# Kernel tuning notes

Measured on AMD Instinct MI355X. Metric: run time of the kernel, lower is better.

Reference implementation:

```python
import jax, jax.numpy as jnp
import numpy as np

N, F, H, O = 3072, 128, 16, 8  # nodes, in_channels, hidden_channels, out_channels


def setup_inputs() -> dict:
    key = jax.random.key(0)
    ks = jax.random.split(key, 8)
    s = 0.01  # xavier gain=0.01 in original init -> small weights
    return {
        "x": jax.random.normal(ks[0], (N, F), dtype=jnp.float32),
        "edge_index": jax.random.randint(ks[1], (2, N * 32), 0, N, dtype=jnp.int64),
        "node_distances": jax.random.uniform(ks[2], (N, N), dtype=jnp.float32),
        "normalization_matrix": jnp.ones((N, N), dtype=jnp.float32),
        # per-feature MLPs fs[f]: Linear(1,H) -> ReLU -> (Dropout p=0) -> Linear(H,O), stacked over F
        "W1": s * jax.random.normal(ks[3], (F, H), dtype=jnp.float32),
        "b1": jnp.zeros((F, H), dtype=jnp.float32),
        "W2": s * jax.random.normal(ks[4], (F, H, O), dtype=jnp.float32),
        "b2": jnp.zeros((F, O), dtype=jnp.float32),
        # rho MLP: Linear(1,H) -> ReLU -> Linear(H,O) (bias=True since is_graph_task=False)
        "rW1": s * jax.random.normal(ks[5], (H,), dtype=jnp.float32),
        "rb1": jnp.zeros((H,), dtype=jnp.float32),
        "rW2": s * jax.random.normal(ks[6], (H, O), dtype=jnp.float32),
        "rb2": jnp.zeros((O,), dtype=jnp.float32),
    }


def reference(x, edge_index, node_distances, normalization_matrix,
              W1, b1, W2, b2, rW1, rb1, rW2, rb2):
    # --- per-feature tiny MLPs, vectorized over the feature axis ---
    # h[n,f,:] = relu(x[n,f] * W1[f] + b1[f])
    h = jax.nn.relu(x[:, :, None] * W1[None, :, :] + b1[None, :, :])  # [N,F,H]
    fx = jnp.einsum('nfh,fho->nfo', h, W2) + b2[None, :, :]           # [N,F,O]
    # sum over features first (commutes with the matmul's F-reduction)
    g = fx.sum(axis=1)                                                 # [N,O]

    # --- rho MLP on normalized pairwise distances ---
    d = node_distances / normalization_matrix                          # [N,N]
    hd = jax.nn.relu(d[:, :, None] * rW1 + rb1)                        # [N,N,H]
    m = jnp.einsum('nmh,ho->nmo', hd, rW2) + rb2                       # [N,N,O]

    # out.T in torch: mf = m_dist_perm @ fx_perm summed over features -> [N,O]
    out = jnp.einsum('nmo,mo->no', m, g)                               # [N,O]
    return out
```

## Files before the change

kernel.cpp:

```cpp
#include <hip/hip_runtime.h>
#include <hip/hip_bf16.h>
#include <math.h>

#define NN 3072
#define FF 128
#define HH 16
#define OO 8

#define MC   1024
#define NCH  3
#define RPB  8

#define OFF_GT   0
#define OFF_KP   24576
#define OFF_ROWS 24600
#define OFF_REF  24872

#define NPB 4

__global__ __launch_bounds__(128) void gnan_g_kernel(
    const float* __restrict__ x,
    const float* __restrict__ W1,
    const float* __restrict__ b1,
    const float* __restrict__ W2,
    const float* __restrict__ b2,
    float* __restrict__ gT)
{
    const int f  = threadIdx.x;
    const int n0 = blockIdx.x * NPB;

    float xv[NPB];
#pragma unroll
    for (int ni = 0; ni < NPB; ++ni)
        xv[ni] = x[(size_t)(n0 + ni) * FF + f];

    const float4 b2a = *reinterpret_cast<const float4*>(b2 + f * OO);
    const float4 b2b = *reinterpret_cast<const float4*>(b2 + f * OO + 4);

    float acc[NPB][OO];
#pragma unroll
    for (int ni = 0; ni < NPB; ++ni) {
        acc[ni][0] = b2a.x; acc[ni][1] = b2a.y; acc[ni][2] = b2a.z; acc[ni][3] = b2a.w;
        acc[ni][4] = b2b.x; acc[ni][5] = b2b.y; acc[ni][6] = b2b.z; acc[ni][7] = b2b.w;
    }

    for (int h = 0; h < HH; ++h) {
        const float w1h = W1[f * HH + h];
        const float b1h = b1[f * HH + h];
        const float4 wa = *reinterpret_cast<const float4*>(W2 + (size_t)(f * HH + h) * OO);
        const float4 wb = *reinterpret_cast<const float4*>(W2 + (size_t)(f * HH + h) * OO + 4);
#pragma unroll
        for (int ni = 0; ni < NPB; ++ni) {
            const float a = fmaxf(fmaf(xv[ni], w1h, b1h), 0.f);
            acc[ni][0] = fmaf(a, wa.x, acc[ni][0]);
            acc[ni][1] = fmaf(a, wa.y, acc[ni][1]);
            acc[ni][2] = fmaf(a, wa.z, acc[ni][2]);
            acc[ni][3] = fmaf(a, wa.w, acc[ni][3]);
            acc[ni][4] = fmaf(a, wb.x, acc[ni][4]);
            acc[ni][5] = fmaf(a, wb.y, acc[ni][5]);
            acc[ni][6] = fmaf(a, wb.z, acc[ni][6]);
            acc[ni][7] = fmaf(a, wb.w, acc[ni][7]);
        }
    }

    __shared__ float wsum[2][OO];
    const int lane = threadIdx.x & 63;
    const int wid  = threadIdx.x >> 6;
#pragma unroll
    for (int ni = 0; ni < NPB; ++ni) {
#pragma unroll
        for (int o = 0; o < OO; ++o) {
#pragma unroll
            for (int off = 32; off > 0; off >>= 1)
                acc[ni][o] += __shfl_down(acc[ni][o], off);
        }
        if (lane == 0) {
#pragma unroll
            for (int o = 0; o < OO; ++o) wsum[wid][o] = acc[ni][o];
        }
        __syncthreads();
        if (threadIdx.x < OO)
            gT[threadIdx.x * NN + (n0 + ni)] = wsum[0][threadIdx.x] + wsum[1][threadIdx.x];
        __syncthreads();
    }
}

__global__ __launch_bounds__(256) void gnan_setup_kernel(
    const float* __restrict__ nd,
    const float* __restrict__ nm,
    const float* __restrict__ rW1,
    const float* __restrict__ rb1,
    const float* __restrict__ rW2,
    const float* __restrict__ rb2,
    float* __restrict__ wsf)
{
    const int t = threadIdx.x;

    float w[HH], b[HH], knee[HH];
#pragma unroll
    for (int h = 0; h < HH; ++h) {
        w[h] = rW1[h];
        b[h] = rb1[h];
        knee[h] = (w[h] != 0.f) ? (-b[h] / w[h]) : INFINITY;
    }

    if (t == 0) {
        wsf[OFF_KP + 0]      = -INFINITY;
        wsf[OFF_KP + HH + 1] =  INFINITY;
    }

    if (t < HH) {
        const float wt = rW1[t], bt = rb1[t];
        const float kt = (wt != 0.f) ? (-bt / wt) : INFINITY;
        int r = 0;
#pragma unroll
        for (int h2 = 0; h2 < HH; ++h2)
            r += (knee[h2] < kt || (knee[h2] == kt && h2 < t)) ? 1 : 0;
        wsf[OFF_KP + 1 + r] = kt;
    }

    if (t < (HH + 1) * OO) {
        const int j = t >> 3, o = t & 7;

        float cAdd = rb2[o];
#pragma unroll
        for (int h = 0; h < HH; ++h)
            if (w[h] == 0.f) cAdd += fmaxf(b[h], 0.f) * rW2[h * OO + o];

        float alpha = 0.f, beta = 0.f;
#pragma unroll
        for (int h = 0; h < HH; ++h) {
            int r = 0;
#pragma unroll
            for (int h2 = 0; h2 < HH; ++h2)
                r += (knee[h2] < knee[h] || (knee[h2] == knee[h] && h2 < h)) ? 1 : 0;
            const bool active = (w[h] > 0.f) ? (r < j)
                              : (w[h] < 0.f ? (r >= j) : false);
            if (active) {
                alpha += w[h] * rW2[h * OO + o];
                beta  += b[h] * rW2[h * OO + o];
            }
        }
        const float betaF = beta + cAdd;
        wsf[OFF_ROWS + j * 16 + o]     = alpha;
        wsf[OFF_ROWS + j * 16 + 8 + o] = betaF;

        const float d00 = nd[0] / nm[0];
        int j0 = 0;
#pragma unroll
        for (int h = 0; h < HH; ++h) j0 += (d00 >= knee[h]) ? 1 : 0;

        if (j == j0) {
            wsf[OFF_REF + 2 + o]  = alpha;
            wsf[OFF_REF + 10 + o] = betaF;
            if (o == 0) {
                float clo = -INFINITY, chi = INFINITY;
#pragma unroll
                for (int h = 0; h < HH; ++h) {
                    if (d00 >= knee[h]) clo = fmaxf(clo, knee[h]);
                    else                chi = fminf(chi, knee[h]);
                }
                wsf[OFF_REF + 0] = clo;
                wsf[OFF_REF + 1] = chi;
            }
        }
    }
}

__global__ __launch_bounds__(512) void gnan_main_kernel(
    const float* __restrict__ nd,
    const float* __restrict__ nm,
    const float* __restrict__ wsf,
    float* __restrict__ out)
{
    __shared__ float gs[OO * MC];
    __shared__ float gsum[OO];

    const int t  = threadIdx.x;
    const int b  = blockIdx.x;
    const int rg = b / NCH;
    const int c  = b % NCH;

    {
        float4*       dst = reinterpret_cast<float4*>(gs);
        const float4* src = reinterpret_cast<const float4*>(wsf + OFF_GT);
        for (int i = t; i < OO * MC / 4; i += 512) {
            const int o  = i >> 8;
            const int mi = i & 255;
            dst[i] = src[o * (NN / 4) + c * (MC / 4) + mi];
        }
    }
    const float clo = wsf[OFF_REF + 0];
    const float chi = wsf[OFF_REF + 1];
    __syncthreads();

    const int wave = t >> 6;
    const int lane = t & 63;

    {
        float s = 0.f;
        for (int i = lane; i < MC; i += 64) s += gs[wave * MC + i];
#pragma unroll
        for (int off = 32; off > 0; off >>= 1) s += __shfl_down(s, off);
        if (lane == 0) gsum[wave] = s;
    }
    __syncthreads();

    const int row = rg * RPB + wave;
    const float* __restrict__ drow = nd + (size_t)row * NN + c * MC;
    const float* __restrict__ nrow = nm + (size_t)row * NN + c * MC;

    float dg[OO], corr[OO];
#pragma unroll
    for (int o = 0; o < OO; ++o) { dg[o] = 0.f; corr[o] = 0.f; }

    for (int it = 0; it < MC / 128; ++it) {
        const int m0 = it * 128 + lane * 2;
        const float2 dv = *reinterpret_cast<const float2*>(drow + m0);
        const float2 nv = *reinterpret_cast<const float2*>(nrow + m0);
        float2 gv[OO];
#pragma unroll
        for (int o = 0; o < OO; ++o)
            gv[o] = *reinterpret_cast<const float2*>(&gs[o * MC + m0]);

#pragma unroll
        for (int k = 0; k < 2; ++k) {
            const float d = __fdividef(k == 0 ? dv.x : dv.y,
                                       k == 0 ? nv.x : nv.y);
            if (d >= clo && d < chi) {
#pragma unroll
                for (int o = 0; o < OO; ++o) {
                    const float g = (k == 0) ? gv[o].x : gv[o].y;
                    dg[o] = fmaf(d, g, dg[o]);
                }
            } else {
                int j = 0;
#pragma unroll
                for (int p = 0; p < HH; ++p)
                    j += (d >= wsf[OFF_KP + 1 + p]) ? 1 : 0;
#pragma unroll
                for (int o = 0; o < OO; ++o) {
                    const float a  = wsf[OFF_ROWS + j * 16 + o];
                    const float bb = wsf[OFF_ROWS + j * 16 + 8 + o];
                    const float g  = (k == 0) ? gv[o].x : gv[o].y;
                    const float v  = fmaf(a, d, bb) - wsf[OFF_REF + 10 + o];
                    corr[o] = fmaf(v, g, corr[o]);
                }
            }
        }
    }

    float val[OO];
#pragma unroll
    for (int o = 0; o < OO; ++o)
        val[o] = fmaf(wsf[OFF_REF + 2 + o], dg[o], corr[o]);
#pragma unroll
    for (int o = 0; o < OO; ++o) {
#pragma unroll
        for (int off = 32; off > 0; off >>= 1)
            val[o] += __shfl_down(val[o], off);
    }
    if (lane == 0) {
#pragma unroll
        for (int o = 0; o < OO; ++o)
            atomicAdd(out + (size_t)row * OO + o,
                      fmaf(wsf[OFF_REF + 10 + o], gsum[o], val[o]));
    }
}

extern "C" void kernel_launch(void* const* d_in, const int* in_sizes, int n_in,
                              void* d_out, int out_size, void* d_ws, size_t ws_size,
                              hipStream_t stream) {
    const float* x   = (const float*)d_in[0];
    const float* nd  = (const float*)d_in[2];
    const float* nm  = (const float*)d_in[3];
    const float* W1  = (const float*)d_in[4];
    const float* b1  = (const float*)d_in[5];
    const float* W2  = (const float*)d_in[6];
    const float* b2  = (const float*)d_in[7];
    const float* rW1 = (const float*)d_in[8];
    const float* rb1 = (const float*)d_in[9];
    const float* rW2 = (const float*)d_in[10];
    const float* rb2 = (const float*)d_in[11];
    float* out = (float*)d_out;
    float* wsf = (float*)d_ws;

    gnan_g_kernel<<<NN / NPB, 128, 0, stream>>>(x, W1, b1, W2, b2, wsf + OFF_GT);
    gnan_setup_kernel<<<1, 256, 0, stream>>>(nd, nm, rW1, rb1, rW2, rb2, wsf);
    hipMemsetAsync(out, 0, (size_t)out_size * sizeof(float), stream);
    gnan_main_kernel<<<(NN / RPB) * NCH, 512, 0, stream>>>(nd, nm, wsf, out);
}
```

Before: 149.9 us.

## Fuse setup and memset into compute kernels, cache piecewise tables in LDS

```diff
diff --git a/kernel.cpp b/kernel.cpp
--- a/kernel.cpp
+++ b/kernel.cpp
@@ -12,9 +12,6 @@
 #define RPB  8
 
 #define OFF_GT   0
-#define OFF_KP   24576
-#define OFF_ROWS 24600
-#define OFF_REF  24872
 
 #define NPB 4
 
@@ -24,10 +21,17 @@
     const float* __restrict__ b1,
     const float* __restrict__ W2,
     const float* __restrict__ b2,
-    float* __restrict__ gT)
+    float* __restrict__ gT,
+    float* __restrict__ out)
 {
     const int f  = threadIdx.x;
     const int n0 = blockIdx.x * NPB;
+
+    {
+        const int gid = blockIdx.x * 128 + threadIdx.x;
+        if (gid < NN * OO / 4)
+            reinterpret_cast<float4*>(out)[gid] = make_float4(0.f, 0.f, 0.f, 0.f);
+    }
 
     float xv[NPB];
 #pragma unroll
@@ -63,7 +67,7 @@
         }
     }
 
-    __shared__ float wsum[2][OO];
+    __shared__ float wsum[NPB][2][OO];
     const int lane = threadIdx.x & 63;
     const int wid  = threadIdx.x >> 6;
 #pragma unroll
@@ -76,105 +80,51 @@
         }
         if (lane == 0) {
 #pragma unroll
-            for (int o = 0; o < OO; ++o) wsum[wid][o] = acc[ni][o];
-        }
-        __syncthreads();
-        if (threadIdx.x < OO)
-            gT[threadIdx.x * NN + (n0 + ni)] = wsum[0][threadIdx.x] + wsum[1][threadIdx.x];
-        __syncthreads();
+            for (int o = 0; o < OO; ++o) wsum[ni][wid][o] = acc[ni][o];
+        }
+    }
+    __syncthreads();
+    if (threadIdx.x < NPB * OO) {
+        const int ni = threadIdx.x >> 3, o = threadIdx.x & 7;
+        gT[o * NN + (n0 + ni)] = wsum[ni][0][o] + wsum[ni][1][o];
     }
 }
 
-__global__ __launch_bounds__(256) void gnan_setup_kernel(
+__device__ __forceinline__ void accum_one(
+    float d, float clo, float chi, const float gk[OO],
+    float dg[OO], float corr[OO],
+    const float* KpS, const float (*rowsS)[16], const float* refB)
+{
+    if (d >= clo && d < chi) {
+#pragma unroll
+        for (int o = 0; o < OO; ++o) dg[o] = fmaf(d, gk[o], dg[o]);
+    } else {
+        int j = 0;
+#pragma unroll
+        for (int p = 0; p < HH; ++p) j += (d >= KpS[1 + p]) ? 1 : 0;
+#pragma unroll
+        for (int o = 0; o < OO; ++o) {
+            const float v = fmaf(rowsS[j][o], d, rowsS[j][8 + o]) - refB[o];
+            corr[o] = fmaf(v, gk[o], corr[o]);
+        }
+    }
+}
+
+__global__ __launch_bounds__(512) void gnan_main_kernel(
     const float* __restrict__ nd,
     const float* __restrict__ nm,
+    const float* __restrict__ wsf,
     const float* __restrict__ rW1,
     const float* __restrict__ rb1,
     const float* __restrict__ rW2,
     const float* __restrict__ rb2,
-    float* __restrict__ wsf)
-{
-    const int t = threadIdx.x;
-
-    float w[HH], b[HH], knee[HH];
-#pragma unroll
-    for (int h = 0; h < HH; ++h) {
-        w[h] = rW1[h];
-        b[h] = rb1[h];
-        knee[h] = (w[h] != 0.f) ? (-b[h] / w[h]) : INFINITY;
-    }
-
-    if (t == 0) {
-        wsf[OFF_KP + 0]      = -INFINITY;
-        wsf[OFF_KP + HH + 1] =  INFINITY;
-    }
-
-    if (t < HH) {
-        const float wt = rW1[t], bt = rb1[t];
-        const float kt = (wt != 0.f) ? (-bt / wt) : INFINITY;
-        int r = 0;
-#pragma unroll
-        for (int h2 = 0; h2 < HH; ++h2)
-            r += (knee[h2] < kt || (knee[h2] == kt && h2 < t)) ? 1 : 0;
-        wsf[OFF_KP + 1 + r] = kt;
-    }
-
-    if (t < (HH + 1) * OO) {
-        const int j = t >> 3, o = t & 7;
-
-        float cAdd = rb2[o];
-#pragma unroll
-        for (int h = 0; h < HH; ++h)
-            if (w[h] == 0.f) cAdd += fmaxf(b[h], 0.f) * rW2[h * OO + o];
-
-        float alpha = 0.f, beta = 0.f;
-#pragma unroll
-        for (int h = 0; h < HH; ++h) {
-            int r = 0;
-#pragma unroll
-            for (int h2 = 0; h2 < HH; ++h2)
-                r += (knee[h2] < knee[h] || (knee[h2] == knee[h] && h2 < h)) ? 1 : 0;
-            const bool active = (w[h] > 0.f) ? (r < j)
-                              : (w[h] < 0.f ? (r >= j) : false);
-            if (active) {
-                alpha += w[h] * rW2[h * OO + o];
-                beta  += b[h] * rW2[h * OO + o];
-            }
-        }
-        const float betaF = beta + cAdd;
-        wsf[OFF_ROWS + j * 16 + o]     = alpha;
-        wsf[OFF_ROWS + j * 16 + 8 + o] = betaF;
-
-        const float d00 = nd[0] / nm[0];
-        int j0 = 0;
-#pragma unroll
-        for (int h = 0; h < HH; ++h) j0 += (d00 >= knee[h]) ? 1 : 0;
-
-        if (j == j0) {
-            wsf[OFF_REF + 2 + o]  = alpha;
-            wsf[OFF_REF + 10 + o] = betaF;
-            if (o == 0) {
-                float clo = -INFINITY, chi = INFINITY;
-#pragma unroll
-                for (int h = 0; h < HH; ++h) {
-                    if (d00 >= knee[h]) clo = fmaxf(clo, knee[h]);
-                    else                chi = fminf(chi, knee[h]);
-                }
-                wsf[OFF_REF + 0] = clo;
-                wsf[OFF_REF + 1] = chi;
-            }
-        }
-    }
-}
-
-__global__ __launch_bounds__(512) void gnan_main_kernel(
-    const float* __restrict__ nd,
-    const float* __restrict__ nm,
-    const float* __restrict__ wsf,
     float* __restrict__ out)
 {
     __shared__ float gs[OO * MC];
     __shared__ float gsum[OO];
+    __shared__ float KpS[HH + 2];
+    __shared__ float rowsS[HH + 1][16];
+    __shared__ float refS[18];
 
     const int t  = threadIdx.x;
     const int b  = blockIdx.x;
@@ -184,14 +134,78 @@
     {
         float4*       dst = reinterpret_cast<float4*>(gs);
         const float4* src = reinterpret_cast<const float4*>(wsf + OFF_GT);
-        for (int i = t; i < OO * MC / 4; i += 512) {
+#pragma unroll
+        for (int r = 0; r < OO * MC / 4 / 512; ++r) {
+            const int i  = r * 512 + t;
             const int o  = i >> 8;
             const int mi = i & 255;
             dst[i] = src[o * (NN / 4) + c * (MC / 4) + mi];
         }
     }
-    const float clo = wsf[OFF_REF + 0];
-    const float chi = wsf[OFF_REF + 1];
+
+    if (t < (HH + 1) * OO + 2) {
+        float w[HH], bb[HH], knee[HH];
+#pragma unroll
+        for (int h = 0; h < HH; ++h) {
+            w[h]  = rW1[h];
+            bb[h] = rb1[h];
+            knee[h] = (w[h] != 0.f) ? (-bb[h] / w[h]) : INFINITY;
+        }
+        if (t >= (HH + 1) * OO) {
+            KpS[(t - (HH + 1) * OO) * (HH + 1)] =
+                (t == (HH + 1) * OO) ? -INFINITY : INFINITY;
+        } else {
+            const int j = t >> 3, o = t & 7;
+            if (o == 0 && j < HH) {
+                int r = 0;
+#pragma unroll
+                for (int h2 = 0; h2 < HH; ++h2)
+                    r += (knee[h2] < knee[j] || (knee[h2] == knee[j] && h2 < j)) ? 1 : 0;
+                KpS[1 + r] = knee[j];
+            }
+            float cAdd = rb2[o];
+#pragma unroll
+            for (int h = 0; h < HH; ++h)
+                if (w[h] == 0.f) cAdd += fmaxf(bb[h], 0.f) * rW2[h * OO + o];
+
+            float alpha = 0.f, beta = 0.f;
+#pragma unroll
+            for (int h = 0; h < HH; ++h) {
+                int r = 0;
+#pragma unroll
+                for (int h2 = 0; h2 < HH; ++h2)
+                    r += (knee[h2] < knee[h] || (knee[h2] == knee[h] && h2 < h)) ? 1 : 0;
+                const bool active = (w[h] > 0.f) ? (r < j)
+                                  : (w[h] < 0.f ? (r >= j) : false);
+                if (active) {
+                    alpha += w[h]  * rW2[h * OO + o];
+                    beta  += bb[h] * rW2[h * OO + o];
+                }
+            }
+            const float betaF = beta + cAdd;
+            rowsS[j][o]     = alpha;
+            rowsS[j][8 + o] = betaF;
+
+            const float d00 = nd[0] / nm[0];
+            int j0 = 0;
+#pragma unroll
+            for (int h = 0; h < HH; ++h) j0 += (d00 >= knee[h]) ? 1 : 0;
+            if (j == j0) {
+                refS[2 + o]  = alpha;
+                refS[10 + o] = betaF;
+                if (o == 0) {
+                    float clo = -INFINITY, chi = INFINITY;
+#pragma unroll
+                    for (int h = 0; h < HH; ++h) {
+                        if (d00 >= knee[h]) clo = fmaxf(clo, knee[h]);
+                        else                chi = fminf(chi, knee[h]);
+                    }
+                    refS[0] = clo;
+                    refS[1] = chi;
+                }
+            }
+        }
+    }
     __syncthreads();
 
     const int wave = t >> 6;
@@ -204,7 +218,10 @@
         for (int off = 32; off > 0; off >>= 1) s += __shfl_down(s, off);
         if (lane == 0) gsum[wave] = s;
     }
-    __syncthreads();
+
+    const float clo = refS[0];
+    const float chi = refS[1];
+    const float* refB = &refS[10];
 
     const int row = rg * RPB + wave;
     const float* __restrict__ drow = nd + (size_t)row * NN + c * MC;
@@ -214,46 +231,45 @@
 #pragma unroll
     for (int o = 0; o < OO; ++o) { dg[o] = 0.f; corr[o] = 0.f; }
 
-    for (int it = 0; it < MC / 128; ++it) {
-        const int m0 = it * 128 + lane * 2;
-        const float2 dv = *reinterpret_cast<const float2*>(drow + m0);
-        const float2 nv = *reinterpret_cast<const float2*>(nrow + m0);
-        float2 gv[OO];
+    for (int it = 0; it < MC / 256; ++it) {
+        const int m0 = it * 256 + lane * 4;
+        const float4 dv = *reinterpret_cast<const float4*>(drow + m0);
+        const float4 nv = *reinterpret_cast<const float4*>(nrow + m0);
+        float4 gv[OO];
 #pragma unroll
         for (int o = 0; o < OO; ++o)
-            gv[o] = *reinterpret_cast<const float2*>(&gs[o * MC + m0]);
-
-#pragma unroll
-        for (int k = 0; k < 2; ++k) {
-            const float d = __fdividef(k == 0 ? dv.x : dv.y,
-                                       k == 0 ? nv.x : nv.y);
-            if (d >= clo && d < chi) {
-#pragma unroll
-                for (int o = 0; o < OO; ++o) {
-                    const float g = (k == 0) ? gv[o].x : gv[o].y;
-                    dg[o] = fmaf(d, g, dg[o]);
-                }
-            } else {
-                int j = 0;
-#pragma unroll
-                for (int p = 0; p < HH; ++p)
-                    j += (d >= wsf[OFF_KP + 1 + p]) ? 1 : 0;
-#pragma unroll
-                for (int o = 0; o < OO; ++o) {
-                    const float a  = wsf[OFF_ROWS + j * 16 + o];
-                    const float bb = wsf[OFF_ROWS + j * 16 + 8 + o];
-                    const float g  = (k == 0) ? gv[o].x : gv[o].y;
-                    const float v  = fmaf(a, d, bb) - wsf[OFF_REF + 10 + o];
-                    corr[o] = fmaf(v, g, corr[o]);
-                }
-            }
+            gv[o] = *reinterpret_cast<const float4*>(&gs[o * MC + m0]);
+
+        {
+            float gk[OO];
+#pragma unroll
+            for (int o = 0; o < OO; ++o) gk[o] = gv[o].x;
+            accum_one(__fdividef(dv.x, nv.x), clo, chi, gk, dg, corr, KpS, rowsS, refB);
+        }
+        {
+            float gk[OO];
+#pragma unroll
+            for (int o = 0; o < OO; ++o) gk[o] = gv[o].y;
+            accum_one(__fdividef(dv.y, nv.y), clo, chi, gk, dg, corr, KpS, rowsS, refB);
+        }
+        {
+            float gk[OO];
+#pragma unroll
+            for (int o = 0; o < OO; ++o) gk[o] = gv[o].z;
+            accum_one(__fdividef(dv.z, nv.z), clo, chi, gk, dg, corr, KpS, rowsS, refB);
+        }
+        {
+            float gk[OO];
+#pragma unroll
+            for (int o = 0; o < OO; ++o) gk[o] = gv[o].w;
+            accum_one(__fdividef(dv.w, nv.w), clo, chi, gk, dg, corr, KpS, rowsS, refB);
         }
     }
 
     float val[OO];
 #pragma unroll
     for (int o = 0; o < OO; ++o)
-        val[o] = fmaf(wsf[OFF_REF + 2 + o], dg[o], corr[o]);
+        val[o] = fmaf(refS[2 + o], dg[o], corr[o]);
 #pragma unroll
     for (int o = 0; o < OO; ++o) {
 #pragma unroll
@@ -264,7 +280,7 @@
 #pragma unroll
         for (int o = 0; o < OO; ++o)
             atomicAdd(out + (size_t)row * OO + o,
-                      fmaf(wsf[OFF_REF + 10 + o], gsum[o], val[o]));
+                      fmaf(refB[o], gsum[o], val[o]));
     }
 }
 
@@ -285,8 +301,8 @@
     float* out = (float*)d_out;
     float* wsf = (float*)d_ws;
 
-    gnan_g_kernel<<<NN / NPB, 128, 0, stream>>>(x, W1, b1, W2, b2, wsf + OFF_GT);
-    gnan_setup_kernel<<<1, 256, 0, stream>>>(nd, nm, rW1, rb1, rW2, rb2, wsf);
-    hipMemsetAsync(out, 0, (size_t)out_size * sizeof(float), stream);
-    gnan_main_kernel<<<(NN / RPB) * NCH, 512, 0, stream>>>(nd, nm, wsf, out);
+    gnan_g_kernel<<<NN / NPB, 128, 0, stream>>>(x, W1, b1, W2, b2,
+                                                wsf + OFF_GT, out);
+    gnan_main_kernel<<<(NN / RPB) * NCH, 512, 0, stream>>>(
+        nd, nm, wsf, rW1, rb1, rW2, rb2, out);
 }
```

Measured after the change: 167.9 us. 12.0% more time.
